# Performance work log

Measured on AMD Instinct MI355X. Metric: run time of the kernel, lower is better.

Reference implementation:

```python
import jax, jax.numpy as jnp
import numpy as np

DIM = 512
DEPTH = 6
HEADS = 8
HD = DIM // HEADS          # head dim = 64
HALF = HD // 4             # rope half_dim = 16
MLP_H = int(DIM * 4.0)
TOKENS = [1, 4, 16, 64]    # CLS, S1, S2, S3
N = sum(TOKENS)            # 85
MAX_FREQ = 10.0
BATCH = 1024
LN_EPS = 1e-5


def _build_mask():
    # CLS sees CLS+S3; each scale sees CLS+itself (block-diagonal + CLS column)
    m = np.full((N, N), -np.inf, dtype=np.float32)
    cum = np.cumsum([0] + TOKENS)  # [0,1,5,21,85]
    m[0, 0] = 0.0
    m[0, cum[3]:cum[4]] = 0.0
    for i in range(1, 4):
        s, e = cum[i], cum[i + 1]
        m[s:e, 0] = 0.0
        m[s:e, s:e] = 0.0
    return jnp.asarray(m)

MASK = _build_mask()
FREQS = jnp.exp(jnp.arange(HALF, dtype=jnp.float32) * (-np.log(MAX_FREQ) / HALF))


def _layer_norm(x, g, b):
    mu = x.mean(-1, keepdims=True)
    var = ((x - mu) ** 2).mean(-1, keepdims=True)
    return (x - mu) * jax.lax.rsqrt(var + LN_EPS) * g + b


def _rope2d(t, coords):
    # t: [B,H,P,HD], coords: [P,2] in [0,1]^2
    ang_x = coords[:, 0:1] * FREQS[None, :] * (2.0 * jnp.pi)  # [P,HALF]
    ang_y = coords[:, 1:2] * FREQS[None, :] * (2.0 * jnp.pi)
    cx, sx = jnp.cos(ang_x), jnp.sin(ang_x)
    cy, sy = jnp.cos(ang_y), jnp.sin(ang_y)
    B, H, P, _ = t.shape
    t = t.reshape(B, H, P, 4, HALF)
    x0, x1, x2, x3 = t[..., 0, :], t[..., 1, :], t[..., 2, :], t[..., 3, :]
    r = jnp.stack([x0 * cx - x1 * sx,
                   x0 * sx + x1 * cx,
                   x2 * cy - x3 * sy,
                   x2 * sy + x3 * cy], axis=3)
    return r.reshape(B, H, P, HD)


def _rope_skip_cls(t, coords):
    return jnp.concatenate([t[:, :, :1], _rope2d(t[:, :, 1:], coords)], axis=2)


def _block(x, coords, p):
    (ln1g, ln1b, qkvw, qkvb, projw, projb,
     ln2g, ln2b, f1w, f1b, f2w, f2b) = p
    B, Nn, D = x.shape
    h = _layer_norm(x, ln1g, ln1b)
    qkv = h @ qkvw + qkvb                         # [B,N,3D]
    qkv = qkv.reshape(B, Nn, 3, HEADS, HD).transpose(2, 0, 3, 1, 4)
    q, k, v = qkv[0], qkv[1], qkv[2]              # [B,H,N,HD]
    q = _rope_skip_cls(q, coords)
    k = _rope_skip_cls(k, coords)
    attn = jnp.einsum('bhqd,bhkd->bhqk', q, k) * (HD ** -0.5) + MASK
    attn = jax.nn.softmax(attn, axis=-1)
    out = jnp.einsum('bhqk,bhkd->bhqd', attn, v)
    out = out.transpose(0, 2, 1, 3).reshape(B, Nn, D)
    x = x + (out @ projw + projb)
    h = _layer_norm(x, ln2g, ln2b)
    h = jax.nn.gelu(h @ f1w + f1b, approximate=False) @ f2w + f2b
    return x + h


def setup_inputs() -> dict:
    key = jax.random.key(0)
    ks = jax.random.split(key, 8)
    s = 0.02
    nrm = lambda k, shape: jax.random.normal(k, shape, jnp.float32) * s
    return dict(
        x=jax.random.normal(ks[0], (BATCH, N, DIM), jnp.float32),
        coords=jax.random.uniform(ks[1], (N - 1, 2), jnp.float32),
        ln1_g=jnp.ones((DEPTH, DIM), jnp.float32),
        ln1_b=jnp.zeros((DEPTH, DIM), jnp.float32),
        qkv_w=nrm(ks[2], (DEPTH, DIM, 3 * DIM)),
        qkv_b=jnp.zeros((DEPTH, 3 * DIM), jnp.float32),
        proj_w=nrm(ks[3], (DEPTH, DIM, DIM)),
        proj_b=jnp.zeros((DEPTH, DIM), jnp.float32),
        ln2_g=jnp.ones((DEPTH, DIM), jnp.float32),
        ln2_b=jnp.zeros((DEPTH, DIM), jnp.float32),
        fc1_w=nrm(ks[4], (DEPTH, DIM, MLP_H)),
        fc1_b=jnp.zeros((DEPTH, MLP_H), jnp.float32),
        fc2_w=nrm(ks[5], (DEPTH, MLP_H, DIM)),
        fc2_b=jnp.zeros((DEPTH, DIM), jnp.float32),
    )


def reference(x, coords, ln1_g, ln1_b, qkv_w, qkv_b, proj_w, proj_b,
              ln2_g, ln2_b, fc1_w, fc1_b, fc2_w, fc2_b):
    for i in range(DEPTH):
        x = _block(x, coords,
                   (ln1_g[i], ln1_b[i], qkv_w[i], qkv_b[i], proj_w[i], proj_b[i],
                    ln2_g[i], ln2_b[i], fc1_w[i], fc1_b[i], fc2_w[i], fc2_b[i]))
    return x
```

## Files before the change

### kernel.cpp

```cpp
#include <hip/hip_runtime.h>
#include <hip/hip_bf16.h>
#include <math.h>

#define DIMX 512
#define NTOK 85
#define BATCH 1024
#define M_ROWS (BATCH * NTOK)
#define MLP_H 2048
#define DEPTH 6

typedef __attribute__((ext_vector_type(8))) short short8;
typedef __attribute__((ext_vector_type(4))) float f32x4;

__device__ inline float bf2f(ushort u) {
    union { unsigned int i; float f; } v; v.i = ((unsigned int)u) << 16; return v.f;
}
__device__ inline ushort f2bf(float f) {
    __hip_bfloat16 h = __float2bfloat16(f);
    union { __hip_bfloat16 h; ushort u; } v; v.h = h; return v.u;
}
__device__ inline unsigned int pack2(float a, float b) {
    return (unsigned int)f2bf(a) | ((unsigned int)f2bf(b) << 16);
}

__device__ inline void gload16(const ushort* g, ushort* lds) {
    __builtin_amdgcn_global_load_lds(
        (const __attribute__((address_space(1))) unsigned int*)g,
        (__attribute__((address_space(3))) unsigned int*)lds, 16, 0, 0);
}

__global__ __launch_bounds__(256) void transpose_bf16(const float* __restrict__ in,
                                                      ushort* __restrict__ out,
                                                      int K, int N) {
    __shared__ float tile[32][33];
    int n0 = blockIdx.x * 32, k0 = blockIdx.y * 32;
    int tx = threadIdx.x, ty = threadIdx.y;
    #pragma unroll
    for (int j = 0; j < 32; j += 8)
        tile[ty + j][tx] = in[(size_t)(k0 + ty + j) * N + n0 + tx];
    __syncthreads();
    #pragma unroll
    for (int j = 0; j < 32; j += 8)
        out[(size_t)(n0 + ty + j) * K + k0 + tx] = f2bf(tile[tx][ty + j]);
}

__global__ void rope_table(const float* __restrict__ coords, float* __restrict__ tab) {
    int t = blockIdx.x;
    int idx = threadIdx.x;
    float freq = expf(-(float)idx * (2.302585093f / 16.0f));
    float twopi = 6.283185307179586f;
    float ax = coords[t * 2 + 0] * freq * twopi;
    float ay = coords[t * 2 + 1] * freq * twopi;
    tab[t * 64 + idx]      = cosf(ax);
    tab[t * 64 + 16 + idx] = sinf(ax);
    tab[t * 64 + 32 + idx] = cosf(ay);
    tab[t * 64 + 48 + idx] = sinf(ay);
}

__global__ __launch_bounds__(256) void ln_kernel(const float* __restrict__ x,
                                                 const float* __restrict__ g,
                                                 const float* __restrict__ bta,
                                                 ushort* __restrict__ out) {
    int w = threadIdx.x >> 6, lane = threadIdx.x & 63;
    size_t row = (size_t)blockIdx.x * 4 + w;
    const float* xr = x + row * DIMX;
    int c = lane * 8;
    float4 v0 = *(const float4*)(xr + c);
    float4 v1 = *(const float4*)(xr + c + 4);
    float s = v0.x + v0.y + v0.z + v0.w + v1.x + v1.y + v1.z + v1.w;
    #pragma unroll
    for (int m = 32; m; m >>= 1) s += __shfl_xor(s, m);
    float mu = s * (1.0f / 512.0f);
    float d0 = v0.x - mu, d1 = v0.y - mu, d2 = v0.z - mu, d3 = v0.w - mu;
    float d4 = v1.x - mu, d5 = v1.y - mu, d6 = v1.z - mu, d7 = v1.w - mu;
    float q = d0*d0 + d1*d1 + d2*d2 + d3*d3 + d4*d4 + d5*d5 + d6*d6 + d7*d7;
    #pragma unroll
    for (int m = 32; m; m >>= 1) q += __shfl_xor(q, m);
    float rs = rsqrtf(q * (1.0f / 512.0f) + 1e-5f);
    float4 g0 = *(const float4*)(g + c), g1 = *(const float4*)(g + c + 4);
    float4 b0 = *(const float4*)(bta + c), b1 = *(const float4*)(bta + c + 4);
    uint4 o;
    o.x = pack2(d0 * rs * g0.x + b0.x, d1 * rs * g0.y + b0.y);
    o.y = pack2(d2 * rs * g0.z + b0.z, d3 * rs * g0.w + b0.w);
    o.z = pack2(d4 * rs * g1.x + b1.x, d5 * rs * g1.y + b1.y);
    o.w = pack2(d6 * rs * g1.z + b1.z, d7 * rs * g1.w + b1.w);
    *(uint4*)&out[row * DIMX + c] = o;
}

template <int EPI>
__global__ __launch_bounds__(256, 4) void gemm_bt(const ushort* __restrict__ A,
                                                  const ushort* __restrict__ Bt,
                                                  const float* __restrict__ bias,
                                                  float* __restrict__ outF,
                                                  ushort* __restrict__ outB,
                                                  int M, int N, int K,
                                                  const float* __restrict__ tab) {
    __shared__ ushort As[2][128 * 32] __attribute__((aligned(16)));
    __shared__ ushort Bs[2][128 * 32] __attribute__((aligned(16)));
    int tid = threadIdx.x;
    int w = tid >> 6, lane = tid & 63;
    int wm = (w >> 1) * 64, wn = (w & 1) * 64;

    int nbx = gridDim.x;
    int nwg = nbx * gridDim.y;
    int orig = blockIdx.y * nbx + blockIdx.x;
    int q8 = nwg >> 3, r8 = nwg & 7;
    int xcd = orig & 7, loc = orig >> 3;
    int id = (xcd < r8) ? xcd * (q8 + 1) + loc : r8 * (q8 + 1) + (xcd - r8) * q8 + loc;
    int m0 = (id / nbx) * 128;
    int n0 = (id % nbx) * 128;

    int srow = tid >> 2;
    int scol = ((tid & 3) ^ ((srow >> 1) & 3)) * 8;
    int ar0 = m0 + srow;      if (ar0 >= M) ar0 = M - 1;
    int ar1 = m0 + 64 + srow; if (ar1 >= M) ar1 = M - 1;
    const ushort* apA0 = A + (size_t)ar0 * K + scol;
    const ushort* apA1 = A + (size_t)ar1 * K + scol;
    const ushort* bpB0 = Bt + (size_t)(n0 + srow) * K + scol;
    const ushort* bpB1 = Bt + (size_t)(n0 + 64 + srow) * K + scol;
    int dP0 = (w * 16) * 32;
    int dP1 = (64 + w * 16) * 32;

    int r = lane & 15, q = lane >> 4;
    int qs = (q ^ ((r >> 1) & 3)) * 8;
    int aoff = (wm + r) * 32 + qs;
    int boff = (wn + r) * 32 + qs;

    int NT = K >> 5;

    #pragma unroll
    for (int t = 0; t < 2; ++t) {
        gload16(apA0 + t * 32, &As[t][dP0]);
        gload16(apA1 + t * 32, &As[t][dP1]);
        gload16(bpB0 + t * 32, &Bs[t][dP0]);
        gload16(bpB1 + t * 32, &Bs[t][dP1]);
    }

    f32x4 acc[4][4] = {};

    for (int t = 0; t < NT; ++t) {
        if (t == NT - 1) asm volatile("s_waitcnt vmcnt(0)" ::: "memory");
        else             asm volatile("s_waitcnt vmcnt(4)" ::: "memory");
        __builtin_amdgcn_s_barrier();
        const ushort* sa = As[t & 1];
        const ushort* sb = Bs[t & 1];
        short8 a[4], b[4];
        #pragma unroll
        for (int i = 0; i < 4; i++) a[i] = *(const short8*)&sa[aoff + i * 512];
        #pragma unroll
        for (int j = 0; j < 4; j++) b[j] = *(const short8*)&sb[boff + j * 512];
        asm volatile("s_waitcnt lgkmcnt(0)" ::: "memory");
        __builtin_amdgcn_sched_barrier(0);
        __builtin_amdgcn_s_barrier();
        if (t + 2 < NT) {
            int kc = (t + 2) * 32;
            gload16(apA0 + kc, &As[t & 1][dP0]);
            gload16(apA1 + kc, &As[t & 1][dP1]);
            gload16(bpB0 + kc, &Bs[t & 1][dP0]);
            gload16(bpB1 + kc, &Bs[t & 1][dP1]);
        }
        __builtin_amdgcn_sched_barrier(0);
        __builtin_amdgcn_s_setprio(1);
        #pragma unroll
        for (int i = 0; i < 4; i++)
            #pragma unroll
            for (int j = 0; j < 4; j++)
                acc[i][j] = __builtin_amdgcn_mfma_f32_16x16x32_bf16(a[i], b[j], acc[i][j], 0, 0, 0);
        __builtin_amdgcn_s_setprio(0);
    }

    int cr = q * 4;
    int cc = r;
    if (EPI == 0) {
        bool ropeReg = (n0 + wn) < 1024;
        int gnb = n0 + wn + cc;
        float bb0 = bias[gnb], bb1 = bias[gnb + 16], bb2 = bias[gnb + 32], bb3 = bias[gnb + 48];
        #pragma unroll
        for (int i = 0; i < 4; i++) {
            #pragma unroll
            for (int rr = 0; rr < 4; rr++) {
                int gm = m0 + wm + i * 16 + cr + rr;
                if (gm >= M) continue;
                int n = gm % NTOK;
                float v0 = acc[i][0][rr] + bb0;
                float v1 = acc[i][1][rr] + bb1;
                float v2 = acc[i][2][rr] + bb2;
                float v3 = acc[i][3][rr] + bb3;
                if (ropeReg && n > 0) {
                    const float* tt = tab + (size_t)(n - 1) * 64 + cc;
                    float cx = tt[0], sx = tt[16], cy = tt[32], sy = tt[48];
                    float y0 = v0 * cx - v1 * sx;
                    float y1 = v0 * sx + v1 * cx;
                    float y2 = v2 * cy - v3 * sy;
                    float y3 = v2 * sy + v3 * cy;
                    v0 = y0; v1 = y1; v2 = y2; v3 = y3;
                }
                size_t o = (size_t)gm * N + gnb;
                outB[o]      = f2bf(v0);
                outB[o + 16] = f2bf(v1);
                outB[o + 32] = f2bf(v2);
                outB[o + 48] = f2bf(v3);
            }
        }
    } else {
        #pragma unroll
        for (int i = 0; i < 4; i++) {
            #pragma unroll
            for (int j = 0; j < 4; j++) {
                #pragma unroll
                for (int rr = 0; rr < 4; rr++) {
                    int gm = m0 + wm + i * 16 + cr + rr;
                    if (gm >= M) continue;
                    int gn = n0 + wn + j * 16 + cc;
                    float v = acc[i][j][rr] + bias[gn];
                    size_t o = (size_t)gm * N + gn;
                    if (EPI == 1) {
                        outF[o] = outF[o] + v;
                    } else {
                        float ge = 0.5f * v * (1.0f + erff(v * 0.70710678118f));
                        outB[o] = f2bf(ge);
                    }
                }
            }
        }
    }
}

__global__ __launch_bounds__(384) void attn_kernel(const ushort* __restrict__ qkv,
                                                   ushort* __restrict__ out) {
    __shared__ ushort SU[13824] __attribute__((aligned(16)));
    __shared__ ushort Vt[6656]  __attribute__((aligned(16)));
    int bh = blockIdx.x;
    int b = bh >> 3, h = bh & 7;
    int tid = threadIdx.x;
    size_t base = (size_t)b * NTOK * 1536 + h * 64;

    for (int it = tid; it < 1536; it += 384) {
        int mat = (it >= 768) ? 1 : 0;
        int item = it - mat * 768;
        int n = item >> 3, g = item & 7;
        short8 v = {};
        if (n < NTOK)
            v = *(const short8*)&qkv[base + (size_t)n * 1536 + mat * 512 + g * 8];
        *(short8*)&SU[mat * 6912 + n * 72 + g * 8] = v;
    }
    for (int it = tid; it < 768; it += 384) {
        int n = it % 96;
        int d0 = (it / 96) * 8;
        short8 v = {};
        if (n < NTOK)
            v = *(const short8*)&qkv[base + (size_t)n * 1536 + 1024 + d0];
        #pragma unroll
        for (int j = 0; j < 8; j++)
            Vt[(d0 + j) * 104 + n] = (ushort)v[j];
    }
    __syncthreads();

    int wid = tid >> 6;
    int lane = tid & 63;
    int q = lane >> 4, c = lane & 15;
    int i0 = wid * 16;

    f32x4 acc[6] = {};
    #pragma unroll
    for (int kk = 0; kk < 2; kk++) {
        short8 aq = *(const short8*)&SU[(i0 + c) * 72 + kk * 32 + q * 8];
        #pragma unroll
        for (int t = 0; t < 6; t++) {
            short8 bk = *(const short8*)&SU[6912 + (t * 16 + c) * 72 + kk * 32 + q * 8];
            acc[t] = __builtin_amdgcn_mfma_f32_16x16x32_bf16(aq, bk, acc[t], 0, 0, 0);
        }
    }
    __syncthreads();

    #pragma unroll
    for (int r = 0; r < 4; r++) {
        int i = i0 + q * 4 + r;
        int si = (i == 0) ? 3 : (i < 5 ? 1 : (i < 21 ? 2 : 3));
        float vs[6];
        float m = -1e30f;
        #pragma unroll
        for (int t = 0; t < 6; t++) {
            int j = t * 16 + c;
            int sj = (j == 0) ? si : (j < 5 ? 1 : (j < 21 ? 2 : (j < NTOK ? 3 : -1)));
            float v = (sj == si) ? acc[t][r] * 0.125f : -1e30f;
            vs[t] = v;
            m = fmaxf(m, v);
        }
        #pragma unroll
        for (int mk = 8; mk; mk >>= 1) m = fmaxf(m, __shfl_xor(m, mk));
        float s = 0.f, ps[6];
        #pragma unroll
        for (int t = 0; t < 6; t++) { ps[t] = __expf(vs[t] - m); s += ps[t]; }
        #pragma unroll
        for (int mk = 8; mk; mk >>= 1) s += __shfl_xor(s, mk);
        float inv = 1.0f / s;
        #pragma unroll
        for (int t = 0; t < 6; t++)
            SU[i * 104 + t * 16 + c] = f2bf(ps[t] * inv);
    }
    __syncthreads();

    f32x4 o2[4] = {};
    #pragma unroll
    for (int kk = 0; kk < 3; kk++) {
        short8 ap = *(const short8*)&SU[(i0 + c) * 104 + kk * 32 + q * 8];
        #pragma unroll
        for (int nt = 0; nt < 4; nt++) {
            short8 bv = *(const short8*)&Vt[(nt * 16 + c) * 104 + kk * 32 + q * 8];
            o2[nt] = __builtin_amdgcn_mfma_f32_16x16x32_bf16(ap, bv, o2[nt], 0, 0, 0);
        }
    }
    size_t orow = (size_t)b * NTOK;
    #pragma unroll
    for (int nt = 0; nt < 4; nt++) {
        #pragma unroll
        for (int r = 0; r < 4; r++) {
            int i = i0 + q * 4 + r;
            if (i < NTOK)
                out[(orow + i) * DIMX + h * 64 + nt * 16 + c] = f2bf(o2[nt][r]);
        }
    }
}

extern "C" void kernel_launch(void* const* d_in, const int* in_sizes, int n_in,
                              void* d_out, int out_size, void* d_ws, size_t ws_size,
                              hipStream_t stream) {
    const float* x_in    = (const float*)d_in[0];
    const float* coords  = (const float*)d_in[1];
    const float* ln1_g   = (const float*)d_in[2];
    const float* ln1_b   = (const float*)d_in[3];
    const float* qkv_w   = (const float*)d_in[4];
    const float* qkv_b   = (const float*)d_in[5];
    const float* proj_w  = (const float*)d_in[6];
    const float* proj_b  = (const float*)d_in[7];
    const float* ln2_g   = (const float*)d_in[8];
    const float* ln2_b   = (const float*)d_in[9];
    const float* fc1_w   = (const float*)d_in[10];
    const float* fc1_b   = (const float*)d_in[11];
    const float* fc2_w   = (const float*)d_in[12];
    const float* fc2_b   = (const float*)d_in[13];

    char* ws = (char*)d_ws;
    size_t off = 0;
    auto alloc = [&](size_t bytes) -> void* {
        void* p = ws + off;
        off += (bytes + 255) & ~(size_t)255;
        return p;
    };
    auto asz = [](size_t b) { return (b + 255) & ~(size_t)255; };

    const size_t WPL = 512 * 1536 + 512 * 512 + 512 * 2048 + 2048 * 512;

    size_t fixed = asz(WPL * DEPTH * sizeof(ushort)) + asz(84 * 64 * sizeof(float));
    int Bc = 1024;
    while (Bc > 4) {
        size_t rc = (size_t)Bc * NTOK;
        size_t need = fixed + asz(rc * DIMX * sizeof(ushort)) + asz(rc * MLP_H * sizeof(ushort));
        if (need <= ws_size) break;
        Bc >>= 1;
    }
    size_t Rc = (size_t)Bc * NTOK;

    ushort* wt   = (ushort*)alloc(WPL * DEPTH * sizeof(ushort));
    float*  tab  = (float*)alloc(84 * 64 * sizeof(float));
    ushort* hbuf = (ushort*)alloc(Rc * DIMX * sizeof(ushort));
    ushort* big  = (ushort*)alloc(Rc * MLP_H * sizeof(ushort));

    hipMemcpyAsync(d_out, x_in, (size_t)M_ROWS * DIMX * sizeof(float),
                   hipMemcpyDeviceToDevice, stream);

    rope_table<<<84, 16, 0, stream>>>(coords, tab);

    dim3 tb(32, 8);
    for (int l = 0; l < DEPTH; l++) {
        ushort* wl = wt + (size_t)l * WPL;
        transpose_bf16<<<dim3(1536 / 32, 512 / 32), tb, 0, stream>>>(
            qkv_w + (size_t)l * 512 * 1536, wl, 512, 1536);
        transpose_bf16<<<dim3(512 / 32, 512 / 32), tb, 0, stream>>>(
            proj_w + (size_t)l * 512 * 512, wl + 786432, 512, 512);
        transpose_bf16<<<dim3(2048 / 32, 512 / 32), tb, 0, stream>>>(
            fc1_w + (size_t)l * 512 * 2048, wl + 1048576, 512, 2048);
        transpose_bf16<<<dim3(512 / 32, 2048 / 32), tb, 0, stream>>>(
            fc2_w + (size_t)l * 2048 * 512, wl + 2097152, 2048, 512);
    }

    int mt = (int)(Rc / 128);
    int lnblocks = (int)(Rc / 4);
    for (int c = 0; c < BATCH / Bc; c++) {
        float* xc = (float*)d_out + (size_t)c * Rc * DIMX;
        int Mc = (int)Rc;
        for (int l = 0; l < DEPTH; l++) {
            ushort* wl = wt + (size_t)l * WPL;
            ln_kernel<<<lnblocks, 256, 0, stream>>>(
                xc, ln1_g + l * 512, ln1_b + l * 512, hbuf);
            gemm_bt<0><<<dim3(1536 / 128, mt), 256, 0, stream>>>(
                hbuf, wl, qkv_b + (size_t)l * 1536, nullptr, big, Mc, 1536, 512, tab);
            attn_kernel<<<Bc * 8, 384, 0, stream>>>(big, hbuf);
            gemm_bt<1><<<dim3(512 / 128, mt), 256, 0, stream>>>(
                hbuf, wl + 786432, proj_b + (size_t)l * 512, xc, nullptr,
                Mc, 512, 512, nullptr);
            ln_kernel<<<lnblocks, 256, 0, stream>>>(
                xc, ln2_g + l * 512, ln2_b + l * 512, hbuf);
            gemm_bt<2><<<dim3(2048 / 128, mt), 256, 0, stream>>>(
                hbuf, wl + 1048576, fc1_b + (size_t)l * 2048, nullptr, big,
                Mc, 2048, 512, nullptr);
            gemm_bt<1><<<dim3(512 / 128, mt), 256, 0, stream>>>(
                big, wl + 2097152, fc2_b + (size_t)l * 512, xc, nullptr,
                Mc, 512, 2048, nullptr);
        }
    }
}
```

Before: 7.834 ms.

## Enlarge GEMM tiles to 256x256 with 8 waves and 4-stage LDS pipeline

Changes the bf16 GEMM from 128x128 tiles with 4 waves and double buffering to 256x256 tiles with 8 waves, each computing 128x64, and a 4-slot prefetch ring staged three tiles ahead. It drops the second barrier per k-step by issuing the next global loads right after the LDS reads. The aim is more operand reuse per loaded byte and deeper latency hiding. The cost is more LDS use (128KB) and more accumulators, which cuts occupancy. The N=512 GEMMs also get far fewer workgroups, and M tiles are rounded up with row clamping.

After: 7.841 ms. About the same (+0.1%).

```diff
diff --git a/kernel.cpp b/kernel.cpp
--- a/kernel.cpp
+++ b/kernel.cpp
@@ -88,18 +88,19 @@
 }
 
 template <int EPI>
-__global__ __launch_bounds__(256, 4) void gemm_bt(const ushort* __restrict__ A,
+__global__ __launch_bounds__(512, 2) void gemm_bt(const ushort* __restrict__ A,
                                                   const ushort* __restrict__ Bt,
                                                   const float* __restrict__ bias,
                                                   float* __restrict__ outF,
                                                   ushort* __restrict__ outB,
                                                   int M, int N, int K,
                                                   const float* __restrict__ tab) {
-    __shared__ ushort As[2][128 * 32] __attribute__((aligned(16)));
-    __shared__ ushort Bs[2][128 * 32] __attribute__((aligned(16)));
+    __shared__ ushort As[4][256 * 32] __attribute__((aligned(16)));
+    __shared__ ushort Bs[4][256 * 32] __attribute__((aligned(16)));
     int tid = threadIdx.x;
     int w = tid >> 6, lane = tid & 63;
-    int wm = (w >> 1) * 64, wn = (w & 1) * 64;
+    int wm2 = (w >> 2) * 128;
+    int wn4 = (w & 3) * 64;
 
     int nbx = gridDim.x;
     int nwg = nbx * gridDim.y;
@@ -107,79 +108,73 @@
     int q8 = nwg >> 3, r8 = nwg & 7;
     int xcd = orig & 7, loc = orig >> 3;
     int id = (xcd < r8) ? xcd * (q8 + 1) + loc : r8 * (q8 + 1) + (xcd - r8) * q8 + loc;
-    int m0 = (id / nbx) * 128;
-    int n0 = (id % nbx) * 128;
-
-    int srow = tid >> 2;
-    int scol = ((tid & 3) ^ ((srow >> 1) & 3)) * 8;
-    int ar0 = m0 + srow;      if (ar0 >= M) ar0 = M - 1;
-    int ar1 = m0 + 64 + srow; if (ar1 >= M) ar1 = M - 1;
-    const ushort* apA0 = A + (size_t)ar0 * K + scol;
-    const ushort* apA1 = A + (size_t)ar1 * K + scol;
-    const ushort* bpB0 = Bt + (size_t)(n0 + srow) * K + scol;
-    const ushort* bpB1 = Bt + (size_t)(n0 + 64 + srow) * K + scol;
-    int dP0 = (w * 16) * 32;
-    int dP1 = (64 + w * 16) * 32;
-
-    int r = lane & 15, q = lane >> 4;
-    int qs = (q ^ ((r >> 1) & 3)) * 8;
-    int aoff = (wm + r) * 32 + qs;
-    int boff = (wn + r) * 32 + qs;
+    int m0 = (id / nbx) * 256;
+    int n0 = (id % nbx) * 256;
+
+    int g1i = tid + 512;
+    int r0 = tid >> 2, r1 = g1i >> 2;
+    int q0 = (tid & 3) ^ ((r0 >> 1) & 3);
+    int q1 = (g1i & 3) ^ ((r1 >> 1) & 3);
+    int ar0 = m0 + r0; if (ar0 >= M) ar0 = M - 1;
+    int ar1 = m0 + r1; if (ar1 >= M) ar1 = M - 1;
+    const ushort* apA0 = A + (size_t)ar0 * K + q0 * 8;
+    const ushort* apA1 = A + (size_t)ar1 * K + q1 * 8;
+    const ushort* bpB0 = Bt + (size_t)(n0 + r0) * K + q0 * 8;
+    const ushort* bpB1 = Bt + (size_t)(n0 + r1) * K + q1 * 8;
+    int d0 = w * 512;
+    int d1 = w * 512 + 4096;
+
+    int l15 = lane & 15, lq = lane >> 4;
+    int sw = (lq ^ ((l15 >> 1) & 3)) * 8;
+    int aoff = (wm2 + l15) * 32 + sw;
+    int boff = (wn4 + l15) * 32 + sw;
 
     int NT = K >> 5;
 
-    #pragma unroll
-    for (int t = 0; t < 2; ++t) {
-        gload16(apA0 + t * 32, &As[t][dP0]);
-        gload16(apA1 + t * 32, &As[t][dP1]);
-        gload16(bpB0 + t * 32, &Bs[t][dP0]);
-        gload16(bpB1 + t * 32, &Bs[t][dP1]);
-    }
-
-    f32x4 acc[4][4] = {};
+#define STAGE(T) do { int kc = (T) * 32, sl = (T) & 3;                      \
+        gload16(apA0 + kc, &As[sl][d0]); gload16(apA1 + kc, &As[sl][d1]);   \
+        gload16(bpB0 + kc, &Bs[sl][d0]); gload16(bpB1 + kc, &Bs[sl][d1]); } while (0)
+
+    STAGE(0); STAGE(1); STAGE(2);
+
+    f32x4 acc[8][4] = {};
 
     for (int t = 0; t < NT; ++t) {
-        if (t == NT - 1) asm volatile("s_waitcnt vmcnt(0)" ::: "memory");
-        else             asm volatile("s_waitcnt vmcnt(4)" ::: "memory");
+        if (t < NT - 2)       asm volatile("s_waitcnt vmcnt(8)" ::: "memory");
+        else if (t == NT - 2) asm volatile("s_waitcnt vmcnt(4)" ::: "memory");
+        else                  asm volatile("s_waitcnt vmcnt(0)" ::: "memory");
         __builtin_amdgcn_s_barrier();
-        const ushort* sa = As[t & 1];
-        const ushort* sb = Bs[t & 1];
-        short8 a[4], b[4];
-        #pragma unroll
-        for (int i = 0; i < 4; i++) a[i] = *(const short8*)&sa[aoff + i * 512];
+        const ushort* sa = As[t & 3];
+        const ushort* sb = Bs[t & 3];
+        short8 a[8], b[4];
+        #pragma unroll
+        for (int i = 0; i < 8; i++) a[i] = *(const short8*)&sa[aoff + i * 512];
         #pragma unroll
         for (int j = 0; j < 4; j++) b[j] = *(const short8*)&sb[boff + j * 512];
+        if (t + 3 < NT) STAGE(t + 3);
         asm volatile("s_waitcnt lgkmcnt(0)" ::: "memory");
         __builtin_amdgcn_sched_barrier(0);
-        __builtin_amdgcn_s_barrier();
-        if (t + 2 < NT) {
-            int kc = (t + 2) * 32;
-            gload16(apA0 + kc, &As[t & 1][dP0]);
-            gload16(apA1 + kc, &As[t & 1][dP1]);
-            gload16(bpB0 + kc, &Bs[t & 1][dP0]);
-            gload16(bpB1 + kc, &Bs[t & 1][dP1]);
-        }
-        __builtin_amdgcn_sched_barrier(0);
         __builtin_amdgcn_s_setprio(1);
         #pragma unroll
-        for (int i = 0; i < 4; i++)
+        for (int i = 0; i < 8; i++)
             #pragma unroll
             for (int j = 0; j < 4; j++)
                 acc[i][j] = __builtin_amdgcn_mfma_f32_16x16x32_bf16(a[i], b[j], acc[i][j], 0, 0, 0);
         __builtin_amdgcn_s_setprio(0);
     }
-
-    int cr = q * 4;
-    int cc = r;
+#undef STAGE
+
+    int cr = lq * 4;
+    int cc = l15;
     if (EPI == 0) {
-        bool ropeReg = (n0 + wn) < 1024;
-        int gnb = n0 + wn + cc;
+        bool ropeReg = (n0 + wn4) < 1024;
+        int gnb = n0 + wn4 + cc;
         float bb0 = bias[gnb], bb1 = bias[gnb + 16], bb2 = bias[gnb + 32], bb3 = bias[gnb + 48];
         #pragma unroll
-        for (int i = 0; i < 4; i++) {
+        for (int i = 0; i < 8; i++) {
             #pragma unroll
             for (int rr = 0; rr < 4; rr++) {
-                int gm = m0 + wm + i * 16 + cr + rr;
+                int gm = m0 + wm2 + i * 16 + cr + rr;
                 if (gm >= M) continue;
                 int n = gm % NTOK;
                 float v0 = acc[i][0][rr] + bb0;
@@ -204,14 +199,14 @@
         }
     } else {
         #pragma unroll
-        for (int i = 0; i < 4; i++) {
+        for (int i = 0; i < 8; i++) {
             #pragma unroll
-            for (int j = 0; j < 4; j++) {
+            for (int rr = 0; rr < 4; rr++) {
+                int gm = m0 + wm2 + i * 16 + cr + rr;
+                if (gm >= M) continue;
                 #pragma unroll
-                for (int rr = 0; rr < 4; rr++) {
-                    int gm = m0 + wm + i * 16 + cr + rr;
-                    if (gm >= M) continue;
-                    int gn = n0 + wn + j * 16 + cc;
+                for (int j = 0; j < 4; j++) {
+                    int gn = n0 + wn4 + j * 16 + cc;
                     float v = acc[i][j][rr] + bias[gn];
                     size_t o = (size_t)gm * N + gn;
                     if (EPI == 1) {
@@ -385,7 +380,7 @@
             fc2_w + (size_t)l * 2048 * 512, wl + 2097152, 2048, 512);
     }
 
-    int mt = (int)(Rc / 128);
+    int mt = (int)((Rc + 255) / 256);
     int lnblocks = (int)(Rc / 4);
     for (int c = 0; c < BATCH / Bc; c++) {
         float* xc = (float*)d_out + (size_t)c * Rc * DIMX;
@@ -394,18 +389,18 @@
             ushort* wl = wt + (size_t)l * WPL;
             ln_kernel<<<lnblocks, 256, 0, stream>>>(
                 xc, ln1_g + l * 512, ln1_b + l * 512, hbuf);
-            gemm_bt<0><<<dim3(1536 / 128, mt), 256, 0, stream>>>(
+            gemm_bt<0><<<dim3(1536 / 256, mt), 512, 0, stream>>>(
                 hbuf, wl, qkv_b + (size_t)l * 1536, nullptr, big, Mc, 1536, 512, tab);
             attn_kernel<<<Bc * 8, 384, 0, stream>>>(big, hbuf);
-            gemm_bt<1><<<dim3(512 / 128, mt), 256, 0, stream>>>(
+            gemm_bt<1><<<dim3(512 / 256, mt), 512, 0, stream>>>(
                 hbuf, wl + 786432, proj_b + (size_t)l * 512, xc, nullptr,
                 Mc, 512, 512, nullptr);
             ln_kernel<<<lnblocks, 256, 0, stream>>>(
                 xc, ln2_g + l * 512, ln2_b + l * 512, hbuf);
-            gemm_bt<2><<<dim3(2048 / 128, mt), 256, 0, stream>>>(
+            gemm_bt<2><<<dim3(2048 / 256, mt), 512, 0, stream>>>(
                 hbuf, wl + 1048576, fc1_b + (size_t)l * 2048, nullptr, big,
                 Mc, 2048, 512, nullptr);
-            gemm_bt<1><<<dim3(512 / 128, mt), 256, 0, stream>>>(
+            gemm_bt<1><<<dim3(512 / 256, mt), 512, 0, stream>>>(
                 big, wl + 2097152, fc2_b + (size_t)l * 512, xc, nullptr,
                 Mc, 512, 2048, nullptr);
         }
```

## Add 256x128-tile GEMM for fc2 and use tanh-form GELU approximation

Applied to the files above, without the earlier changes.

Adds a gemm_wide kernel with 256x128 output tiles (8x4 MFMA fragments per wave), double-buffered LDS loads and XCD-aware block remapping. It is used for the fc2 GEMM (K=2048) to raise data reuse per loaded tile and reduce global traffic. It also replaces the erf-based GELU in the fc1 epilogue with a sigmoid/tanh approximation using __expf. The larger tile raises register pressure, and the GELU change adds a small numerical deviation from the exact erf form.

Result: faster. 7.502 ms (-4.2%).

```diff
diff --git a/kernel.cpp b/kernel.cpp
--- a/kernel.cpp
+++ b/kernel.cpp
@@ -21,6 +21,10 @@
 }
 __device__ inline unsigned int pack2(float a, float b) {
     return (unsigned int)f2bf(a) | ((unsigned int)f2bf(b) << 16);
+}
+__device__ inline float gelu_fast(float v) {
+    float u = 1.5957691f * fmaf(0.044715f * v, v * v, v);
+    return v / (1.0f + __expf(-u));
 }
 
 __device__ inline void gload16(const ushort* g, ushort* lds) {
@@ -217,8 +221,146 @@
                     if (EPI == 1) {
                         outF[o] = outF[o] + v;
                     } else {
-                        float ge = 0.5f * v * (1.0f + erff(v * 0.70710678118f));
-                        outB[o] = f2bf(ge);
+                        outB[o] = f2bf(gelu_fast(v));
+                    }
+                }
+            }
+        }
+    }
+}
+
+template <int EPI>
+__global__ __launch_bounds__(256, 2) void gemm_wide(const ushort* __restrict__ A,
+                                                    const ushort* __restrict__ Bt,
+                                                    const float* __restrict__ bias,
+                                                    float* __restrict__ outF,
+                                                    ushort* __restrict__ outB,
+                                                    int M, int N, int K,
+                                                    const float* __restrict__ tab) {
+    __shared__ ushort As[2][256 * 32] __attribute__((aligned(16)));
+    __shared__ ushort Bs[2][128 * 32] __attribute__((aligned(16)));
+    int tid = threadIdx.x;
+    int w = tid >> 6, lane = tid & 63;
+    int wm2 = (w >> 1) * 128;
+    int wn = (w & 1) * 64;
+
+    int nbx = gridDim.x;
+    int nwg = nbx * gridDim.y;
+    int orig = blockIdx.y * nbx + blockIdx.x;
+    int q8 = nwg >> 3, r8 = nwg & 7;
+    int xcd = orig & 7, loc = orig >> 3;
+    int id = (xcd < r8) ? xcd * (q8 + 1) + loc : r8 * (q8 + 1) + (xcd - r8) * q8 + loc;
+    int m0 = (id / nbx) * 256;
+    int n0 = (id % nbx) * 128;
+
+    int srow = tid >> 2;
+    int scol = ((tid & 3) ^ ((srow >> 1) & 3)) * 8;
+    const ushort* gAp[4];
+    const ushort* gBp[2];
+    #pragma unroll
+    for (int rn = 0; rn < 4; rn++) {
+        int rr2 = m0 + srow + rn * 64; if (rr2 >= M) rr2 = M - 1;
+        gAp[rn] = A + (size_t)rr2 * K + scol;
+    }
+    #pragma unroll
+    for (int rn = 0; rn < 2; rn++)
+        gBp[rn] = Bt + (size_t)(n0 + srow + rn * 64) * K + scol;
+    int dwz = w * 512;
+
+#define STAGEW(T) do { int kc = (T) * 32, sl = (T) & 1;                        \
+        gload16(gAp[0] + kc, &As[sl][dwz]);                                    \
+        gload16(gAp[1] + kc, &As[sl][2048 + dwz]);                             \
+        gload16(gAp[2] + kc, &As[sl][4096 + dwz]);                             \
+        gload16(gAp[3] + kc, &As[sl][6144 + dwz]);                             \
+        gload16(gBp[0] + kc, &Bs[sl][dwz]);                                    \
+        gload16(gBp[1] + kc, &Bs[sl][2048 + dwz]); } while (0)
+
+    int l15 = lane & 15, lq = lane >> 4;
+    int sw = (lq ^ ((l15 >> 1) & 3)) * 8;
+    int aoff = (wm2 + l15) * 32 + sw;
+    int boff = (wn + l15) * 32 + sw;
+
+    int NT = K >> 5;
+
+    STAGEW(0); STAGEW(1);
+
+    f32x4 acc[8][4] = {};
+
+    for (int t = 0; t < NT; ++t) {
+        if (t == NT - 1) asm volatile("s_waitcnt vmcnt(0)" ::: "memory");
+        else             asm volatile("s_waitcnt vmcnt(6)" ::: "memory");
+        __builtin_amdgcn_s_barrier();
+        const ushort* sa = As[t & 1];
+        const ushort* sb = Bs[t & 1];
+        short8 a[8], b[4];
+        #pragma unroll
+        for (int i = 0; i < 8; i++) a[i] = *(const short8*)&sa[aoff + i * 512];
+        #pragma unroll
+        for (int j = 0; j < 4; j++) b[j] = *(const short8*)&sb[boff + j * 512];
+        asm volatile("s_waitcnt lgkmcnt(0)" ::: "memory");
+        __builtin_amdgcn_sched_barrier(0);
+        __builtin_amdgcn_s_barrier();
+        if (t + 2 < NT) STAGEW(t + 2);
+        __builtin_amdgcn_sched_barrier(0);
+        __builtin_amdgcn_s_setprio(1);
+        #pragma unroll
+        for (int i = 0; i < 8; i++)
+            #pragma unroll
+            for (int j = 0; j < 4; j++)
+                acc[i][j] = __builtin_amdgcn_mfma_f32_16x16x32_bf16(a[i], b[j], acc[i][j], 0, 0, 0);
+        __builtin_amdgcn_s_setprio(0);
+    }
+#undef STAGEW
+
+    int cr = lq * 4;
+    int cc = l15;
+    if (EPI == 0) {
+        bool ropeReg = (n0 + wn) < 1024;
+        int gnb = n0 + wn + cc;
+        float bb0 = bias[gnb], bb1 = bias[gnb + 16], bb2 = bias[gnb + 32], bb3 = bias[gnb + 48];
+        #pragma unroll
+        for (int i = 0; i < 8; i++) {
+            #pragma unroll
+            for (int rr = 0; rr < 4; rr++) {
+                int gm = m0 + wm2 + i * 16 + cr + rr;
+                if (gm >= M) continue;
+                int n = gm % NTOK;
+                float v0 = acc[i][0][rr] + bb0;
+                float v1 = acc[i][1][rr] + bb1;
+                float v2 = acc[i][2][rr] + bb2;
+                float v3 = acc[i][3][rr] + bb3;
+                if (ropeReg && n > 0) {
+                    const float* tt = tab + (size_t)(n - 1) * 64 + cc;
+                    float cx = tt[0], sx = tt[16], cy = tt[32], sy = tt[48];
+                    float y0 = v0 * cx - v1 * sx;
+                    float y1 = v0 * sx + v1 * cx;
+                    float y2 = v2 * cy - v3 * sy;
+                    float y3 = v2 * sy + v3 * cy;
+                    v0 = y0; v1 = y1; v2 = y2; v3 = y3;
+                }
+                size_t o = (size_t)gm * N + gnb;
+                outB[o]      = f2bf(v0);
+                outB[o + 16] = f2bf(v1);
+                outB[o + 32] = f2bf(v2);
+                outB[o + 48] = f2bf(v3);
+            }
+        }
+    } else {
+        #pragma unroll
+        for (int i = 0; i < 8; i++) {
+            #pragma unroll
+            for (int rr = 0; rr < 4; rr++) {
+                int gm = m0 + wm2 + i * 16 + cr + rr;
+                if (gm >= M) continue;
+                #pragma unroll
+                for (int j = 0; j < 4; j++) {
+                    int gn = n0 + wn + j * 16 + cc;
+                    float v = acc[i][j][rr] + bias[gn];
+                    size_t o = (size_t)gm * N + gn;
+                    if (EPI == 1) {
+                        outF[o] = outF[o] + v;
+                    } else {
+                        outB[o] = f2bf(gelu_fast(v));
                     }
                 }
             }
@@ -385,7 +527,8 @@
             fc2_w + (size_t)l * 2048 * 512, wl + 2097152, 2048, 512);
     }
 
-    int mt = (int)(Rc / 128);
+    int mt128 = (int)(Rc / 128);
+    int mt256 = (int)(Rc / 256);
     int lnblocks = (int)(Rc / 4);
     for (int c = 0; c < BATCH / Bc; c++) {
         float* xc = (float*)d_out + (size_t)c * Rc * DIMX;
@@ -394,18 +537,18 @@
             ushort* wl = wt + (size_t)l * WPL;
             ln_kernel<<<lnblocks, 256, 0, stream>>>(
                 xc, ln1_g + l * 512, ln1_b + l * 512, hbuf);
-            gemm_bt<0><<<dim3(1536 / 128, mt), 256, 0, stream>>>(
+            gemm_bt<0><<<dim3(1536 / 128, mt128), 256, 0, stream>>>(
                 hbuf, wl, qkv_b + (size_t)l * 1536, nullptr, big, Mc, 1536, 512, tab);
             attn_kernel<<<Bc * 8, 384, 0, stream>>>(big, hbuf);
-            gemm_bt<1><<<dim3(512 / 128, mt), 256, 0, stream>>>(
+            gemm_bt<1><<<dim3(512 / 128, mt128), 256, 0, stream>>>(
                 hbuf, wl + 786432, proj_b + (size_t)l * 512, xc, nullptr,
                 Mc, 512, 512, nullptr);
             ln_kernel<<<lnblocks, 256, 0, stream>>>(
                 xc, ln2_g + l * 512, ln2_b + l * 512, hbuf);
-            gemm_bt<2><<<dim3(2048 / 128, mt), 256, 0, stream>>>(
+            gemm_bt<2><<<dim3(2048 / 128, mt128), 256, 0, stream>>>(
                 hbuf, wl + 1048576, fc1_b + (size_t)l * 2048, nullptr, big,
                 Mc, 2048, 512, nullptr);
-            gemm_bt<1><<<dim3(512 / 128, mt), 256, 0, stream>>>(
+            gemm_wide<1><<<dim3(512 / 128, mt256), 256, 0, stream>>>(
                 big, wl + 2097152, fc2_b + (size_t)l * 512, xc, nullptr,
                 Mc, 512, 2048, nullptr);
         }
```
